# Kernel tuning notes

Hardware: AMD Instinct MI355X
Metric: run time of the kernel (lower is better)

Reference implementation:

```python
import jax, jax.numpy as jnp
import numpy as np

B, T, C = 2, 192, 512
H, D = 8, 64  # num_heads, head_dim; inner_dim = H*D = C


def setup_inputs() -> dict:
    key = jax.random.key(0)
    k1, k2, k3 = jax.random.split(key, 3)
    x = jax.random.normal(k1, (B, T, C), dtype=jnp.float32)
    W_in = jax.random.normal(k2, (C, 5 * H * D), dtype=jnp.float32) * 0.02
    b_in = jnp.zeros((5 * H * D,), dtype=jnp.float32)
    W_out = jax.random.normal(k3, (H * D, C), dtype=jnp.float32) * 0.02
    b_out = jnp.zeros((C,), dtype=jnp.float32)
    return {"x": x, "W_in": W_in, "b_in": b_in, "W_out": W_out, "b_out": b_out}


def _split_heads(t):
    # (B,T,H*D) -> (B,H,T,D)
    return t.reshape(B, T, H, D).transpose(0, 2, 1, 3)


def reference(x, W_in, b_in, W_out, b_out):
    scale = D ** -0.5
    proj = x @ W_in + b_in  # (B,T,5*H*D)
    q, k1, v1, k2, v2 = jnp.split(proj, 5, axis=-1)
    q = _split_heads(q) * scale
    k1 = _split_heads(k1)
    v1 = _split_heads(v1)
    k2 = _split_heads(k2)
    v2 = _split_heads(v2)
    # trilinear logits: <q_i, k1_j, k2_k> / sqrt(D), computed in fp32
    logits = jnp.einsum('bhid,bhjd,bhkd->bhijk', q, k1, k2,
                        preferred_element_type=jnp.float32)
    # softmax over the joint (j,k) axes
    attn = jax.nn.softmax(logits.reshape(B, H, T, T * T), axis=-1)
    attn = attn.reshape(B, H, T, T, T).astype(x.dtype)
    # out_i[d] = sum_{j,k} attn[i,j,k] * v1_j[d] * v2_k[d]
    out = jnp.einsum('bhijk,bhjd,bhkd->bhid', attn, v1, v2)
    y = out.transpose(0, 2, 1, 3).reshape(B, T, H * D)  # merge heads
    return y @ W_out + b_out
```

## Files before the change

kernel.cpp:

```cpp
#include <hip/hip_runtime.h>
#include <hip/hip_bf16.h>


typedef float  v4f __attribute__((ext_vector_type(4)));
typedef short  v8s __attribute__((ext_vector_type(8)));

__device__ __forceinline__ unsigned short f2bf(float f) {
  unsigned u = __float_as_uint(f);
  u += 0x7fffu + ((u >> 16) & 1u);
  return (unsigned short)(u >> 16);
}
__device__ __forceinline__ float bf2f(unsigned short b) {
  return __uint_as_float(((unsigned)b) << 16);
}
__device__ __forceinline__ unsigned pack_bf16(float lo, float hi) {
  __hip_bfloat162 t = __float22bfloat162_rn(float2{lo, hi});
  union { __hip_bfloat162 b; unsigned u; } cv;
  cv.b = t;
  return cv.u;
}

#if __has_builtin(__builtin_amdgcn_exp2f)
#define EXP2F(x) __builtin_amdgcn_exp2f(x)
#else
#define EXP2F(x) exp2f(x)
#endif

#define MFMA32(a, b, c) __builtin_amdgcn_mfma_f32_16x16x32_bf16((a), (b), (c), 0, 0, 0)

#define QSCALE 0.18033688011112042f


#define XH_OFF   589824
#define XL_OFF   786432
#define WTH_OFF  983040
#define WTL_OFF  2293760
#define WOTH_OFF 3604480
#define WOTL_OFF 3866624
#define OH_OFF   4128768
#define OL_OFF   4325376

__device__ __forceinline__ int v1perm(int t) {
  return (t & ~31) | (((t >> 2) & 3) << 3) | (((t >> 4) & 1) << 2) | (t & 3);
}

__global__ __launch_bounds__(256) void prep_kernel(
    const float* __restrict__ x, const float* __restrict__ Win,
    const float* __restrict__ Wout, unsigned short* __restrict__ wsh) {
  __shared__ float tile[32 * 65];
  const int bi = blockIdx.x, t = threadIdx.x;
  if (bi < 768) {
    const float* W; unsigned short *Th, *Tl; int R, n0, k0;
    if (bi < 640) {
      W = Win; Th = wsh + WTH_OFF; Tl = wsh + WTL_OFF; R = 2560;
      n0 = (bi % 40) << 6; k0 = (bi / 40) << 5;
    } else {
      const int idx = bi - 640;
      W = Wout; Th = wsh + WOTH_OFF; Tl = wsh + WOTL_OFF; R = 512;
      n0 = (idx & 7) << 6; k0 = (idx >> 3) << 5;
    }
    const int n = t & 63, kq = (t >> 6) * 8;
#pragma unroll
    for (int j = 0; j < 8; ++j)
      tile[(kq + j) * 65 + n] = W[(k0 + kq + j) * R + n0 + n];
    __syncthreads();
    const int n2 = t >> 2, ks = (t & 3) * 8;
    union { uint4 u; unsigned short us[8]; } ph, pl;
#pragma unroll
    for (int j = 0; j < 8; ++j) {
      const float v = tile[(ks + j) * 65 + n2];
      const unsigned short h = f2bf(v);
      ph.us[j] = h;
      pl.us[j] = f2bf(v - bf2f(h));
    }
    *(uint4*)(Th + (n0 + n2) * 512 + k0 + ks) = ph.u;
    *(uint4*)(Tl + (n0 + n2) * 512 + k0 + ks) = pl.u;
  } else {
    const int flat = ((bi - 768) * 256 + t) * 8;
    const v4f v0 = *(const v4f*)(x + flat);
    const v4f v1 = *(const v4f*)(x + flat + 4);
    union { uint4 u; unsigned short us[8]; } ph, pl;
#pragma unroll
    for (int j = 0; j < 4; ++j) {
      unsigned short h = f2bf(v0[j]);
      ph.us[j] = h; pl.us[j] = f2bf(v0[j] - bf2f(h));
      h = f2bf(v1[j]);
      ph.us[4 + j] = h; pl.us[4 + j] = f2bf(v1[j] - bf2f(h));
    }
    *(uint4*)(wsh + XH_OFF + flat) = ph.u;
    *(uint4*)(wsh + XL_OFF + flat) = pl.u;
  }
}

__global__ __launch_bounds__(64) void proj_kernel(
    const unsigned short* __restrict__ wsh, const float* __restrict__ bin,
    float* __restrict__ wsf, unsigned short* __restrict__ wshd) {
  const int lane = threadIdx.x;
  const int c = lane & 15, q = lane >> 4;
  const int bm = blockIdx.x % 12, bn = blockIdx.x / 12;

  const unsigned short* base[8];
  base[0] = wsh + XH_OFF + (bm * 32 + c) * 512 + (q << 3);
  base[1] = base[0] + 16 * 512;
  base[2] = wsh + XL_OFF + (bm * 32 + c) * 512 + (q << 3);
  base[3] = base[2] + 16 * 512;
  base[4] = wsh + WTH_OFF + (bn * 32 + c) * 512 + (q << 3);
  base[5] = base[4] + 16 * 512;
  base[6] = wsh + WTL_OFF + (bn * 32 + c) * 512 + (q << 3);
  base[7] = base[6] + 16 * 512;

  const v4f z = {0.f, 0.f, 0.f, 0.f};
  v4f a00 = z, a01 = z, a10 = z, a11 = z;

  v8s cur[8], nxt[8];
#pragma unroll
  for (int i = 0; i < 8; ++i) cur[i] = *(const v8s*)(base[i]);
#pragma unroll
  for (int i = 0; i < 8; ++i) nxt[i] = *(const v8s*)(base[i] + 32);

#pragma unroll 1
  for (int ks = 0; ks < 16; ++ks) {
    v8s nx2[8];
    if (ks < 14) {
      const int o = (ks + 2) * 32;
#pragma unroll
      for (int i = 0; i < 8; ++i) nx2[i] = *(const v8s*)(base[i] + o);
    }
    a00 = MFMA32(cur[2], cur[4], a00); a00 = MFMA32(cur[0], cur[6], a00); a00 = MFMA32(cur[0], cur[4], a00);
    a01 = MFMA32(cur[2], cur[5], a01); a01 = MFMA32(cur[0], cur[7], a01); a01 = MFMA32(cur[0], cur[5], a01);
    a10 = MFMA32(cur[3], cur[4], a10); a10 = MFMA32(cur[1], cur[6], a10); a10 = MFMA32(cur[1], cur[4], a10);
    a11 = MFMA32(cur[3], cur[5], a11); a11 = MFMA32(cur[1], cur[7], a11); a11 = MFMA32(cur[1], cur[5], a11);
#pragma unroll
    for (int i = 0; i < 8; ++i) { cur[i] = nxt[i]; nxt[i] = nx2[i]; }
  }

  v4f accs[2][2] = {{a00, a01}, {a10, a11}};
#pragma unroll
  for (int mt = 0; mt < 2; ++mt) {
#pragma unroll
    for (int nt = 0; nt < 2; ++nt) {
      const int n = bn * 32 + nt * 16 + c;
      const int which = n >> 9, cc = n & 511, h = cc >> 6, d = cc & 63;
      const float bv = bin[n];
#pragma unroll
      for (int r = 0; r < 4; ++r) {
        const int m = bm * 32 + mt * 16 + (q << 2) + r;
        const int b = (m >= 192) ? 1 : 0;
        const int tt = m - (b ? 192 : 0);
        const int bh = b * 8 + h;
        const float val = accs[mt][nt][r] + bv;
        const int rm = ((bh * 192 + tt) << 6) + d;
        if (which == 0)      wsf[rm] = val * QSCALE;
        else if (which == 1) wshd[rm] = f2bf(val);
        else if (which == 2) wshd[393216 + ((bh << 6) + d) * 192 + v1perm(tt)] = f2bf(val);
        else if (which == 3) wshd[196608 + rm] = f2bf(val);
        else wsf[196608 + ((bh * 192 + tt) << 6) + ((d >> 4) << 4) + (d & 15)] = val;
      }
    }
  }
}

__global__ __launch_bounds__(256, 2) void attn_kernel(
    const float* __restrict__ wsf, const unsigned short* __restrict__ wsh,
    float* __restrict__ accp, float* __restrict__ Sp) {
  __shared__ char smem[17408];
  unsigned short* K2s = (unsigned short*)smem;

  const int tid  = threadIdx.x;
  const int wv   = tid >> 6;
  const int lane = tid & 63;
  const int c    = lane & 15;
  const int quad = lane >> 4;
  const int jh   = wv & 1;
  const int kh   = wv >> 1;

  const int bb = blockIdx.x;
  const int kb = bb & 3;
  const int it = (bb >> 2) % 12;
  const int bh = bb / 48;

  const unsigned short* k1g = wsh + bh * 192 * 64;
  const unsigned short* v1g = wsh + 393216 + bh * 64 * 192;
  const unsigned short* k2g = wsh + 196608 + bh * 192 * 64;
  const float*          v2g = wsf + 196608 + bh * 12288;

  for (int idx = tid; idx < 384; idx += 256) {
    const int r = idx >> 3, c8 = (idx & 7) * 8;
    *(uint4*)(K2s + r * 64 + c8) = *(const uint4*)(k2g + (kb * 48 + r) * 64 + c8);
  }

  v8s k1f[6][2];
#pragma unroll
  for (int j = 0; j < 6; ++j) {
    const unsigned short* kp = k1g + (((jh * 6 + j) * 16 + c) << 6) + (quad << 3);
    k1f[j][0] = *(const v8s*)(kp);
    k1f[j][1] = *(const v8s*)(kp + 32);
  }

  v8s vf[3][4];
#pragma unroll
  for (int m = 0; m < 3; ++m)
#pragma unroll
    for (int dt = 0; dt < 4; ++dt)
      vf[m][dt] = *(const v8s*)(v1g + (dt * 16 + c) * 192 + ((jh * 3 + m) << 5) + (quad << 3));

  const float* qg = wsf + ((bh * 192 + it * 16 + c) << 6) + (quad << 3);
  float q0[8], q1[8];
  {
    v4f qa = *(const v4f*)(qg), qb = *(const v4f*)(qg + 4);
    v4f qc = *(const v4f*)(qg + 32), qd = *(const v4f*)(qg + 36);
#pragma unroll
    for (int e = 0; e < 4; ++e) {
      q0[e] = qa[e]; q0[4 + e] = qb[e];
      q1[e] = qc[e]; q1[4 + e] = qd[e];
    }
  }
  __syncthreads();

  const v4f z = {0.f, 0.f, 0.f, 0.f};
  v4f acc[4] = {z, z, z, z};
  float sS = 0.f;

  union U4 { uint4 u4; unsigned short us[8]; };
  union AF { v8s v; unsigned u[4]; };

#pragma unroll 1
  for (int ks = 0; ks < 24; ++ks) {
    const int rl = kh * 24 + ks;
    U4 kl, khh;
    kl.u4  = *(const uint4*)(K2s + (rl << 6) + (quad << 3));
    khh.u4 = *(const uint4*)(K2s + (rl << 6) + (quad << 3) + 32);
    const float* vb = v2g + ((kb * 48 + rl) << 6) + (quad << 2);
    const v4f vt0 = *(const v4f*)(vb);
    const v4f vt1 = *(const v4f*)(vb + 16);
    const v4f vt2 = *(const v4f*)(vb + 32);
    const v4f vt3 = *(const v4f*)(vb + 48);

    AF af0, af1;
#pragma unroll
    for (int e = 0; e < 4; ++e) {
      af0.u[e] = pack_bf16(q0[2*e] * bf2f(kl.us[2*e]),  q0[2*e+1] * bf2f(kl.us[2*e+1]));
      af1.u[e] = pack_bf16(q1[2*e] * bf2f(khh.us[2*e]), q1[2*e+1] * bf2f(khh.us[2*e+1]));
    }

    v4f o0 = z, o1 = z, o2 = z, o3 = z;
#pragma unroll
    for (int m = 0; m < 3; ++m) {
      v4f Ca = MFMA32(k1f[2*m][0],   af0.v, z);
      Ca = MFMA32(k1f[2*m][1],   af1.v, Ca);
      v4f Cb = MFMA32(k1f[2*m+1][0], af0.v, z);
      Cb = MFMA32(k1f[2*m+1][1], af1.v, Cb);
#pragma unroll
      for (int r = 0; r < 4; ++r) { Ca[r] = EXP2F(Ca[r]); Cb[r] = EXP2F(Cb[r]); }
      sS += Ca[0] + Ca[1] + Ca[2] + Ca[3] + Cb[0] + Cb[1] + Cb[2] + Cb[3];
      AF pp;
      pp.u[0] = pack_bf16(Ca[0], Ca[1]);
      pp.u[1] = pack_bf16(Ca[2], Ca[3]);
      pp.u[2] = pack_bf16(Cb[0], Cb[1]);
      pp.u[3] = pack_bf16(Cb[2], Cb[3]);
      o0 = MFMA32(vf[m][0], pp.v, o0);
      o1 = MFMA32(vf[m][1], pp.v, o1);
      o2 = MFMA32(vf[m][2], pp.v, o2);
      o3 = MFMA32(vf[m][3], pp.v, o3);
    }
    acc[0] += o0 * vt0;
    acc[1] += o1 * vt1;
    acc[2] += o2 * vt2;
    acc[3] += o3 * vt3;
  }

  __syncthreads();
  float* redA = (float*)smem;
  float* redS = (float*)smem + 4096;

#pragma unroll
  for (int dt = 0; dt < 4; ++dt)
    *(v4f*)(redA + wv * 1024 + (c << 6) + (dt << 4) + (quad << 2)) = acc[dt];
  redS[wv * 64 + (quad << 4) + c] = sS;
  __syncthreads();

  const int pbase = (bh * 12 + it) * 4 + kb;
  float* ap_out = accp + pbase * 1024;
  for (int idx = tid; idx < 1024; idx += 256)
    ap_out[idx] = redA[idx] + redA[1024 + idx] + redA[2048 + idx] + redA[3072 + idx];
  if (tid < 16) {
    float s = 0.f;
#pragma unroll
    for (int w = 0; w < 4; ++w)
#pragma unroll
      for (int qq = 0; qq < 4; ++qq)
        s += redS[w * 64 + qq * 16 + tid];
    Sp[pbase * 16 + tid] = s;
  }
}

__global__ __launch_bounds__(256) void norm_kernel(
    const float* __restrict__ accp, const float* __restrict__ Sp,
    unsigned short* __restrict__ wsh) {
  const int flat = blockIdx.x * 2048 + threadIdx.x * 8;
  const int m = flat >> 9, cc = flat & 511;
  const int b = (m >= 192) ? 1 : 0;
  const int tt = m - (b ? 192 : 0);
  const int h = cc >> 6, d0 = cc & 63;
  const int bh = b * 8 + h, it = tt >> 4, i = tt & 15;
  const int pb = (bh * 12 + it) * 4;
  const float* ap = accp + pb * 1024 + (i << 6) + d0;
  v4f a0 = *(const v4f*)(ap), a1 = *(const v4f*)(ap + 4);
  float Sv = Sp[pb * 16 + i];
#pragma unroll
  for (int kb = 1; kb < 4; ++kb) {
    a0 += *(const v4f*)(ap + kb * 1024);
    a1 += *(const v4f*)(ap + kb * 1024 + 4);
    Sv += Sp[(pb + kb) * 16 + i];
  }
  const float inv = 1.0f / Sv;
  union { uint4 u; unsigned short us[8]; } ph, pl;
#pragma unroll
  for (int j = 0; j < 4; ++j) {
    float v = a0[j] * inv;
    unsigned short hh = f2bf(v);
    ph.us[j] = hh; pl.us[j] = f2bf(v - bf2f(hh));
    v = a1[j] * inv;
    hh = f2bf(v);
    ph.us[4 + j] = hh; pl.us[4 + j] = f2bf(v - bf2f(hh));
  }
  *(uint4*)(wsh + OH_OFF + flat) = ph.u;
  *(uint4*)(wsh + OL_OFF + flat) = pl.u;
}

__global__ __launch_bounds__(64) void outp_kernel(
    const unsigned short* __restrict__ wsh, const float* __restrict__ bout,
    float* __restrict__ y) {
  const int lane = threadIdx.x;
  const int c = lane & 15, q = lane >> 4;
  const int bm = blockIdx.x % 12, bn = blockIdx.x / 12;

  const unsigned short* base[8];
  base[0] = wsh + OH_OFF + (bm * 32 + c) * 512 + (q << 3);
  base[1] = base[0] + 16 * 512;
  base[2] = wsh + OL_OFF + (bm * 32 + c) * 512 + (q << 3);
  base[3] = base[2] + 16 * 512;
  base[4] = wsh + WOTH_OFF + (bn * 32 + c) * 512 + (q << 3);
  base[5] = base[4] + 16 * 512;
  base[6] = wsh + WOTL_OFF + (bn * 32 + c) * 512 + (q << 3);
  base[7] = base[6] + 16 * 512;

  const v4f z = {0.f, 0.f, 0.f, 0.f};
  v4f a00 = z, a01 = z, a10 = z, a11 = z;

  v8s cur[8], nxt[8];
#pragma unroll
  for (int i = 0; i < 8; ++i) cur[i] = *(const v8s*)(base[i]);
#pragma unroll
  for (int i = 0; i < 8; ++i) nxt[i] = *(const v8s*)(base[i] + 32);

#pragma unroll 1
  for (int ks = 0; ks < 16; ++ks) {
    v8s nx2[8];
    if (ks < 14) {
      const int o = (ks + 2) * 32;
#pragma unroll
      for (int i = 0; i < 8; ++i) nx2[i] = *(const v8s*)(base[i] + o);
    }
    a00 = MFMA32(cur[2], cur[4], a00); a00 = MFMA32(cur[0], cur[6], a00); a00 = MFMA32(cur[0], cur[4], a00);
    a01 = MFMA32(cur[2], cur[5], a01); a01 = MFMA32(cur[0], cur[7], a01); a01 = MFMA32(cur[0], cur[5], a01);
    a10 = MFMA32(cur[3], cur[4], a10); a10 = MFMA32(cur[1], cur[6], a10); a10 = MFMA32(cur[1], cur[4], a10);
    a11 = MFMA32(cur[3], cur[5], a11); a11 = MFMA32(cur[1], cur[7], a11); a11 = MFMA32(cur[1], cur[5], a11);
#pragma unroll
    for (int i = 0; i < 8; ++i) { cur[i] = nxt[i]; nxt[i] = nx2[i]; }
  }

  v4f accs[2][2] = {{a00, a01}, {a10, a11}};
#pragma unroll
  for (int mt = 0; mt < 2; ++mt) {
#pragma unroll
    for (int nt = 0; nt < 2; ++nt) {
      const int n = bn * 32 + nt * 16 + c;
      const float bv = bout[n];
#pragma unroll
      for (int r = 0; r < 4; ++r) {
        const int m = bm * 32 + mt * 16 + (q << 2) + r;
        y[m * 512 + n] = accs[mt][nt][r] + bv;
      }
    }
  }
}

extern "C" void kernel_launch(void* const* d_in, const int* in_sizes, int n_in,
                              void* d_out, int out_size, void* d_ws, size_t ws_size,
                              hipStream_t stream) {
  const float* x    = (const float*)d_in[0];
  const float* Win  = (const float*)d_in[1];
  const float* bin  = (const float*)d_in[2];
  const float* Wout = (const float*)d_in[3];
  const float* bout = (const float*)d_in[4];

  float* wsf = (float*)d_ws;
  unsigned short* wsh = (unsigned short*)(wsf + 1191936);
  float* accp = wsf + 393216;
  float* Sp   = wsf + 1179648;

  prep_kernel<<<dim3(864), 256, 0, stream>>>(x, Win, Wout, wsh);
  proj_kernel<<<dim3(960), 64, 0, stream>>>(wsh, bin, wsf, wsh);
  attn_kernel<<<dim3(768), 256, 0, stream>>>(wsf, wsh, accp, Sp);
  norm_kernel<<<dim3(96), 256, 0, stream>>>(accp, Sp, wsh);
  outp_kernel<<<dim3(192), 64, 0, stream>>>(wsh, bout, (float*)d_out);
}
```

Measured before the change: 143.8 us.

## Stage projection epilogue through LDS, pre-convert K2 to fp32, sum softmax via MFMA

The projection epilogue now writes accumulators into a shared tile and stores coalesced vector rows, including a transposed and permuted V1 layout, instead of scattered scalar stores. The attention kernel converts K2 to fp32 once when staging it in shared memory, which removes the per-iteration bf16 unpack. It also computes the softmax denominator with an MFMA against a ones vector, replacing the VALU adds and the 4-way quad reduction. The trade-offs are twice the LDS traffic for K2, a softmax sum taken from bf16-rounded probabilities, and more live registers from restructuring all six logit tiles before the PV MFMAs.

```diff
diff --git a/kernel.cpp b/kernel.cpp
--- a/kernel.cpp
+++ b/kernel.cpp
@@ -40,8 +40,8 @@
 #define OH_OFF   4128768
 #define OL_OFF   4325376
 
-__device__ __forceinline__ int v1perm(int t) {
-  return (t & ~31) | (((t >> 2) & 3) << 3) | (((t >> 4) & 1) << 2) | (t & 3);
+__device__ __forceinline__ int v1perm_inv(int p) {
+  return (((p >> 3) & 3) << 2) | (((p >> 2) & 1) << 4) | (p & 3);
 }
 
 __global__ __launch_bounds__(256) void prep_kernel(
@@ -95,6 +95,7 @@
 __global__ __launch_bounds__(64) void proj_kernel(
     const unsigned short* __restrict__ wsh, const float* __restrict__ bin,
     float* __restrict__ wsf, unsigned short* __restrict__ wshd) {
+  __shared__ float tile[32 * 33];
   const int lane = threadIdx.x;
   const int c = lane & 15, q = lane >> 4;
   const int bm = blockIdx.x % 12, bn = blockIdx.x / 12;
@@ -134,28 +135,58 @@
     for (int i = 0; i < 8; ++i) { cur[i] = nxt[i]; nxt[i] = nx2[i]; }
   }
 
+  const int n0 = bn * 32;
+  const int which = n0 >> 9;
+  const int h  = (n0 & 511) >> 6;
+  const int d0 = n0 & 63;
+  const int b  = (bm >= 6) ? 1 : 0;
+  const int bh = b * 8 + h;
+  const int tt0 = (bm - b * 6) * 32;
+
   v4f accs[2][2] = {{a00, a01}, {a10, a11}};
 #pragma unroll
-  for (int mt = 0; mt < 2; ++mt) {
+  for (int mt = 0; mt < 2; ++mt)
 #pragma unroll
     for (int nt = 0; nt < 2; ++nt) {
-      const int n = bn * 32 + nt * 16 + c;
-      const int which = n >> 9, cc = n & 511, h = cc >> 6, d = cc & 63;
-      const float bv = bin[n];
-#pragma unroll
-      for (int r = 0; r < 4; ++r) {
-        const int m = bm * 32 + mt * 16 + (q << 2) + r;
-        const int b = (m >= 192) ? 1 : 0;
-        const int tt = m - (b ? 192 : 0);
-        const int bh = b * 8 + h;
-        const float val = accs[mt][nt][r] + bv;
-        const int rm = ((bh * 192 + tt) << 6) + d;
-        if (which == 0)      wsf[rm] = val * QSCALE;
-        else if (which == 1) wshd[rm] = f2bf(val);
-        else if (which == 2) wshd[393216 + ((bh << 6) + d) * 192 + v1perm(tt)] = f2bf(val);
-        else if (which == 3) wshd[196608 + rm] = f2bf(val);
-        else wsf[196608 + ((bh * 192 + tt) << 6) + ((d >> 4) << 4) + (d & 15)] = val;
+      const float bv = bin[n0 + nt * 16 + c];
+#pragma unroll
+      for (int r = 0; r < 4; ++r)
+        tile[(mt * 16 + (q << 2) + r) * 33 + nt * 16 + c] = accs[mt][nt][r] + bv;
+    }
+  __syncthreads();
+
+  const int rr = lane >> 1, cc0 = (lane & 1) * 16;
+  if (which == 0 || which == 4) {
+    float* out = wsf + (which == 4 ? 196608 : 0) + ((bh * 192 + tt0 + rr) << 6) + d0 + cc0;
+    const float s = (which == 0) ? QSCALE : 1.0f;
+#pragma unroll
+    for (int i = 0; i < 16; i += 4) {
+      v4f v;
+#pragma unroll
+      for (int j = 0; j < 4; ++j) v[j] = tile[rr * 33 + cc0 + i + j] * s;
+      *(v4f*)(out + i) = v;
+    }
+  } else if (which == 1 || which == 3) {
+    unsigned short* out = wshd + (which == 3 ? 196608 : 0) + ((bh * 192 + tt0 + rr) << 6) + d0 + cc0;
+#pragma unroll
+    for (int hf = 0; hf < 2; ++hf) {
+      union { uint4 u; unsigned short us[8]; } pk;
+#pragma unroll
+      for (int j = 0; j < 8; ++j) pk.us[j] = f2bf(tile[rr * 33 + cc0 + hf * 8 + j]);
+      *(uint4*)(out + hf * 8) = pk.u;
+    }
+  } else {
+    const int dd = rr, p0 = cc0;
+    unsigned short* out = wshd + 393216 + ((bh << 6) + d0 + dd) * 192 + tt0 + p0;
+#pragma unroll
+    for (int hf = 0; hf < 2; ++hf) {
+      union { uint4 u; unsigned short us[8]; } pk;
+#pragma unroll
+      for (int j = 0; j < 8; ++j) {
+        const int p = p0 + hf * 8 + j;
+        pk.us[j] = f2bf(tile[v1perm_inv(p) * 33 + dd]);
       }
+      *(uint4*)(out + hf * 8) = pk.u;
     }
   }
 }
@@ -164,7 +195,7 @@
     const float* __restrict__ wsf, const unsigned short* __restrict__ wsh,
     float* __restrict__ accp, float* __restrict__ Sp) {
   __shared__ char smem[17408];
-  unsigned short* K2s = (unsigned short*)smem;
+  float* K2f = (float*)smem;
 
   const int tid  = threadIdx.x;
   const int wv   = tid >> 6;
@@ -186,7 +217,13 @@
 
   for (int idx = tid; idx < 384; idx += 256) {
     const int r = idx >> 3, c8 = (idx & 7) * 8;
-    *(uint4*)(K2s + r * 64 + c8) = *(const uint4*)(k2g + (kb * 48 + r) * 64 + c8);
+    union { uint4 u4; unsigned short us[8]; } t;
+    t.u4 = *(const uint4*)(k2g + (kb * 48 + r) * 64 + c8);
+    v4f lo, hi;
+#pragma unroll
+    for (int e = 0; e < 4; ++e) { lo[e] = bf2f(t.us[e]); hi[e] = bf2f(t.us[4 + e]); }
+    *(v4f*)(K2f + r * 64 + c8)     = lo;
+    *(v4f*)(K2f + r * 64 + c8 + 4) = hi;
   }
 
   v8s k1f[6][2];
@@ -219,17 +256,20 @@
 
   const v4f z = {0.f, 0.f, 0.f, 0.f};
   v4f acc[4] = {z, z, z, z};
-  float sS = 0.f;
-
-  union U4 { uint4 u4; unsigned short us[8]; };
+  v4f oS = z;
+  const short one = (short)0x3F80;
+  const v8s ones = {one, one, one, one, one, one, one, one};
+
   union AF { v8s v; unsigned u[4]; };
 
 #pragma unroll 1
   for (int ks = 0; ks < 24; ++ks) {
     const int rl = kh * 24 + ks;
-    U4 kl, khh;
-    kl.u4  = *(const uint4*)(K2s + (rl << 6) + (quad << 3));
-    khh.u4 = *(const uint4*)(K2s + (rl << 6) + (quad << 3) + 32);
+    const float* kp = K2f + (rl << 6) + (quad << 3);
+    const v4f k2a = *(const v4f*)(kp);
+    const v4f k2b = *(const v4f*)(kp + 4);
+    const v4f k2c = *(const v4f*)(kp + 32);
+    const v4f k2d = *(const v4f*)(kp + 36);
     const float* vb = v2g + ((kb * 48 + rl) << 6) + (quad << 2);
     const v4f vt0 = *(const v4f*)(vb);
     const v4f vt1 = *(const v4f*)(vb + 16);
@@ -237,31 +277,42 @@
     const v4f vt3 = *(const v4f*)(vb + 48);
 
     AF af0, af1;
-#pragma unroll
-    for (int e = 0; e < 4; ++e) {
-      af0.u[e] = pack_bf16(q0[2*e] * bf2f(kl.us[2*e]),  q0[2*e+1] * bf2f(kl.us[2*e+1]));
-      af1.u[e] = pack_bf16(q1[2*e] * bf2f(khh.us[2*e]), q1[2*e+1] * bf2f(khh.us[2*e+1]));
-    }
-
+    af0.u[0] = pack_bf16(q0[0] * k2a[0], q0[1] * k2a[1]);
+    af0.u[1] = pack_bf16(q0[2] * k2a[2], q0[3] * k2a[3]);
+    af0.u[2] = pack_bf16(q0[4] * k2b[0], q0[5] * k2b[1]);
+    af0.u[3] = pack_bf16(q0[6] * k2b[2], q0[7] * k2b[3]);
+    af1.u[0] = pack_bf16(q1[0] * k2c[0], q1[1] * k2c[1]);
+    af1.u[1] = pack_bf16(q1[2] * k2c[2], q1[3] * k2c[3]);
+    af1.u[2] = pack_bf16(q1[4] * k2d[0], q1[5] * k2d[1]);
+    af1.u[3] = pack_bf16(q1[6] * k2d[2], q1[7] * k2d[3]);
+
+    v4f C[6];
+#pragma unroll
+    for (int jj = 0; jj < 6; ++jj) {
+      v4f t0 = MFMA32(k1f[jj][0], af0.v, z);
+      C[jj] = MFMA32(k1f[jj][1], af1.v, t0);
+    }
+#pragma unroll
+    for (int jj = 0; jj < 6; ++jj)
+#pragma unroll
+      for (int r = 0; r < 4; ++r) C[jj][r] = EXP2F(C[jj][r]);
+    AF pp[3];
+#pragma unroll
+    for (int m = 0; m < 3; ++m) {
+      pp[m].u[0] = pack_bf16(C[2*m][0],   C[2*m][1]);
+      pp[m].u[1] = pack_bf16(C[2*m][2],   C[2*m][3]);
+      pp[m].u[2] = pack_bf16(C[2*m+1][0], C[2*m+1][1]);
+      pp[m].u[3] = pack_bf16(C[2*m+1][2], C[2*m+1][3]);
+    }
+#pragma unroll
+    for (int m = 0; m < 3; ++m) oS = MFMA32(ones, pp[m].v, oS);
     v4f o0 = z, o1 = z, o2 = z, o3 = z;
 #pragma unroll
     for (int m = 0; m < 3; ++m) {
-      v4f Ca = MFMA32(k1f[2*m][0],   af0.v, z);
-      Ca = MFMA32(k1f[2*m][1],   af1.v, Ca);
-      v4f Cb = MFMA32(k1f[2*m+1][0], af0.v, z);
-      Cb = MFMA32(k1f[2*m+1][1], af1.v, Cb);
-#pragma unroll
-      for (int r = 0; r < 4; ++r) { Ca[r] = EXP2F(Ca[r]); Cb[r] = EXP2F(Cb[r]); }
-      sS += Ca[0] + Ca[1] + Ca[2] + Ca[3] + Cb[0] + Cb[1] + Cb[2] + Cb[3];
-      AF pp;
-      pp.u[0] = pack_bf16(Ca[0], Ca[1]);
-      pp.u[1] = pack_bf16(Ca[2], Ca[3]);
-      pp.u[2] = pack_bf16(Cb[0], Cb[1]);
-      pp.u[3] = pack_bf16(Cb[2], Cb[3]);
-      o0 = MFMA32(vf[m][0], pp.v, o0);
-      o1 = MFMA32(vf[m][1], pp.v, o1);
-      o2 = MFMA32(vf[m][2], pp.v, o2);
-      o3 = MFMA32(vf[m][3], pp.v, o3);
+      o0 = MFMA32(vf[m][0], pp[m].v, o0);
+      o1 = MFMA32(vf[m][1], pp[m].v, o1);
+      o2 = MFMA32(vf[m][2], pp[m].v, o2);
+      o3 = MFMA32(vf[m][3], pp[m].v, o3);
     }
     acc[0] += o0 * vt0;
     acc[1] += o1 * vt1;
@@ -276,22 +327,15 @@
 #pragma unroll
   for (int dt = 0; dt < 4; ++dt)
     *(v4f*)(redA + wv * 1024 + (c << 6) + (dt << 4) + (quad << 2)) = acc[dt];
-  redS[wv * 64 + (quad << 4) + c] = sS;
+  if (quad == 0) redS[wv * 16 + c] = oS[0];
   __syncthreads();
 
   const int pbase = (bh * 12 + it) * 4 + kb;
   float* ap_out = accp + pbase * 1024;
   for (int idx = tid; idx < 1024; idx += 256)
     ap_out[idx] = redA[idx] + redA[1024 + idx] + redA[2048 + idx] + redA[3072 + idx];
-  if (tid < 16) {
-    float s = 0.f;
-#pragma unroll
-    for (int w = 0; w < 4; ++w)
-#pragma unroll
-      for (int qq = 0; qq < 4; ++qq)
-        s += redS[w * 64 + qq * 16 + tid];
-    Sp[pbase * 16 + tid] = s;
-  }
+  if (tid < 16)
+    Sp[pbase * 16 + tid] = redS[tid] + redS[16 + tid] + redS[32 + tid] + redS[48 + tid];
 }
 
 __global__ __launch_bounds__(256) void norm_kernel(
```

Result: no change. 146.5 us (+1.9%).

## Fuse softmax normalization into output projection and coalesce projection epilogue stores

Applied to the files above, without the earlier changes.

Merges the separate normalization kernel into the output-projection GEMM: each block reduces the partial accumulators, divides by the softmax denominator, splits into bf16 hi/lo in shared memory, then runs MFMAs against Wout. This removes one launch and the global round trip for the normalized activations, at the cost of fewer, larger blocks (48). The projection epilogue now stages its tile in shared memory so Q/K/V writes (including the permuted V1 transpose) become vectorized, coalesced stores instead of scattered scalar ones. The attention inner loop unroll is raised to 2.

```diff
diff --git a/kernel.cpp b/kernel.cpp
--- a/kernel.cpp
+++ b/kernel.cpp
@@ -37,11 +37,9 @@
 #define WTL_OFF  2293760
 #define WOTH_OFF 3604480
 #define WOTL_OFF 3866624
-#define OH_OFF   4128768
-#define OL_OFF   4325376
-
-__device__ __forceinline__ int v1perm(int t) {
-  return (t & ~31) | (((t >> 2) & 3) << 3) | (((t >> 4) & 1) << 2) | (t & 3);
+
+__device__ __forceinline__ int v1perm_inv(int p) {
+  return (((p >> 3) & 3) << 2) | (((p >> 2) & 1) << 4) | (p & 3);
 }
 
 __global__ __launch_bounds__(256) void prep_kernel(
@@ -95,6 +93,7 @@
 __global__ __launch_bounds__(64) void proj_kernel(
     const unsigned short* __restrict__ wsh, const float* __restrict__ bin,
     float* __restrict__ wsf, unsigned short* __restrict__ wshd) {
+  __shared__ float tile[32 * 33];
   const int lane = threadIdx.x;
   const int c = lane & 15, q = lane >> 4;
   const int bm = blockIdx.x % 12, bn = blockIdx.x / 12;
@@ -134,28 +133,58 @@
     for (int i = 0; i < 8; ++i) { cur[i] = nxt[i]; nxt[i] = nx2[i]; }
   }
 
+  const int n0 = bn * 32;
+  const int which = n0 >> 9;
+  const int h  = (n0 & 511) >> 6;
+  const int d0 = n0 & 63;
+  const int b  = (bm >= 6) ? 1 : 0;
+  const int bh = b * 8 + h;
+  const int tt0 = (bm - b * 6) * 32;
+
   v4f accs[2][2] = {{a00, a01}, {a10, a11}};
 #pragma unroll
-  for (int mt = 0; mt < 2; ++mt) {
+  for (int mt = 0; mt < 2; ++mt)
 #pragma unroll
     for (int nt = 0; nt < 2; ++nt) {
-      const int n = bn * 32 + nt * 16 + c;
-      const int which = n >> 9, cc = n & 511, h = cc >> 6, d = cc & 63;
-      const float bv = bin[n];
-#pragma unroll
-      for (int r = 0; r < 4; ++r) {
-        const int m = bm * 32 + mt * 16 + (q << 2) + r;
-        const int b = (m >= 192) ? 1 : 0;
-        const int tt = m - (b ? 192 : 0);
-        const int bh = b * 8 + h;
-        const float val = accs[mt][nt][r] + bv;
-        const int rm = ((bh * 192 + tt) << 6) + d;
-        if (which == 0)      wsf[rm] = val * QSCALE;
-        else if (which == 1) wshd[rm] = f2bf(val);
-        else if (which == 2) wshd[393216 + ((bh << 6) + d) * 192 + v1perm(tt)] = f2bf(val);
-        else if (which == 3) wshd[196608 + rm] = f2bf(val);
-        else wsf[196608 + ((bh * 192 + tt) << 6) + ((d >> 4) << 4) + (d & 15)] = val;
+      const float bv = bin[n0 + nt * 16 + c];
+#pragma unroll
+      for (int r = 0; r < 4; ++r)
+        tile[(mt * 16 + (q << 2) + r) * 33 + nt * 16 + c] = accs[mt][nt][r] + bv;
+    }
+  __syncthreads();
+
+  const int rr = lane >> 1, cc0 = (lane & 1) * 16;
+  if (which == 0 || which == 4) {
+    float* out = wsf + (which == 4 ? 196608 : 0) + ((bh * 192 + tt0 + rr) << 6) + d0 + cc0;
+    const float s = (which == 0) ? QSCALE : 1.0f;
+#pragma unroll
+    for (int i = 0; i < 16; i += 4) {
+      v4f v;
+#pragma unroll
+      for (int j = 0; j < 4; ++j) v[j] = tile[rr * 33 + cc0 + i + j] * s;
+      *(v4f*)(out + i) = v;
+    }
+  } else if (which == 1 || which == 3) {
+    unsigned short* out = wshd + (which == 3 ? 196608 : 0) + ((bh * 192 + tt0 + rr) << 6) + d0 + cc0;
+#pragma unroll
+    for (int hf = 0; hf < 2; ++hf) {
+      union { uint4 u; unsigned short us[8]; } pk;
+#pragma unroll
+      for (int j = 0; j < 8; ++j) pk.us[j] = f2bf(tile[rr * 33 + cc0 + hf * 8 + j]);
+      *(uint4*)(out + hf * 8) = pk.u;
+    }
+  } else {
+    const int dd = rr, p0 = cc0;
+    unsigned short* out = wshd + 393216 + ((bh << 6) + d0 + dd) * 192 + tt0 + p0;
+#pragma unroll
+    for (int hf = 0; hf < 2; ++hf) {
+      union { uint4 u; unsigned short us[8]; } pk;
+#pragma unroll
+      for (int j = 0; j < 8; ++j) {
+        const int p = p0 + hf * 8 + j;
+        pk.us[j] = f2bf(tile[v1perm_inv(p) * 33 + dd]);
       }
+      *(uint4*)(out + hf * 8) = pk.u;
     }
   }
 }
@@ -224,7 +253,7 @@
   union U4 { uint4 u4; unsigned short us[8]; };
   union AF { v8s v; unsigned u[4]; };
 
-#pragma unroll 1
+#pragma unroll 2
   for (int ks = 0; ks < 24; ++ks) {
     const int rl = kh * 24 + ks;
     U4 kl, khh;
@@ -294,95 +323,91 @@
   }
 }
 
-__global__ __launch_bounds__(256) void norm_kernel(
-    const float* __restrict__ accp, const float* __restrict__ Sp,
-    unsigned short* __restrict__ wsh) {
-  const int flat = blockIdx.x * 2048 + threadIdx.x * 8;
-  const int m = flat >> 9, cc = flat & 511;
-  const int b = (m >= 192) ? 1 : 0;
-  const int tt = m - (b ? 192 : 0);
-  const int h = cc >> 6, d0 = cc & 63;
-  const int bh = b * 8 + h, it = tt >> 4, i = tt & 15;
-  const int pb = (bh * 12 + it) * 4;
-  const float* ap = accp + pb * 1024 + (i << 6) + d0;
-  v4f a0 = *(const v4f*)(ap), a1 = *(const v4f*)(ap + 4);
-  float Sv = Sp[pb * 16 + i];
-#pragma unroll
-  for (int kb = 1; kb < 4; ++kb) {
-    a0 += *(const v4f*)(ap + kb * 1024);
-    a1 += *(const v4f*)(ap + kb * 1024 + 4);
-    Sv += Sp[(pb + kb) * 16 + i];
-  }
-  const float inv = 1.0f / Sv;
-  union { uint4 u; unsigned short us[8]; } ph, pl;
-#pragma unroll
-  for (int j = 0; j < 4; ++j) {
-    float v = a0[j] * inv;
-    unsigned short hh = f2bf(v);
-    ph.us[j] = hh; pl.us[j] = f2bf(v - bf2f(hh));
-    v = a1[j] * inv;
-    hh = f2bf(v);
-    ph.us[4 + j] = hh; pl.us[4 + j] = f2bf(v - bf2f(hh));
-  }
-  *(uint4*)(wsh + OH_OFF + flat) = ph.u;
-  *(uint4*)(wsh + OL_OFF + flat) = pl.u;
-}
-
-__global__ __launch_bounds__(64) void outp_kernel(
-    const unsigned short* __restrict__ wsh, const float* __restrict__ bout,
-    float* __restrict__ y) {
-  const int lane = threadIdx.x;
+__global__ __launch_bounds__(256) void outp2_kernel(
+    const float* __restrict__ wsf, const unsigned short* __restrict__ wsh,
+    const float* __restrict__ bout, float* __restrict__ y) {
+  __shared__ unsigned short OHs[16 * 520];
+  __shared__ unsigned short OLs[16 * 520];
+  const float* accp = wsf + 393216;
+  const float* Sp   = wsf + 1179648;
+
+  const int tid = threadIdx.x;
+  const int nh  = blockIdx.x & 1;
+  const int bit = blockIdx.x >> 1;
+  const int b = bit / 12, it = bit % 12;
+  const int m0 = b * 192 + it * 16;
+
+  {
+    const int i = tid >> 4, cc0 = (tid & 15) * 32;
+    const int h = cc0 >> 6;
+    const int pb = ((b * 8 + h) * 12 + it) * 4;
+    const float inv = 1.0f / (Sp[pb * 16 + i] + Sp[(pb + 1) * 16 + i] +
+                              Sp[(pb + 2) * 16 + i] + Sp[(pb + 3) * 16 + i]);
+    const float* ap = accp + pb * 1024 + (i << 6) + (cc0 & 63);
+#pragma unroll
+    for (int g = 0; g < 8; ++g) {
+      v4f a = *(const v4f*)(ap + g * 4);
+      a += *(const v4f*)(ap + 1024 + g * 4);
+      a += *(const v4f*)(ap + 2048 + g * 4);
+      a += *(const v4f*)(ap + 3072 + g * 4);
+#pragma unroll
+      for (int j = 0; j < 4; ++j) {
+        const float v = a[j] * inv;
+        const unsigned short hh = f2bf(v);
+        OHs[i * 520 + cc0 + g * 4 + j] = hh;
+        OLs[i * 520 + cc0 + g * 4 + j] = f2bf(v - bf2f(hh));
+      }
+    }
+  }
+  __syncthreads();
+
+  const int lane = tid & 63, wv = tid >> 6;
   const int c = lane & 15, q = lane >> 4;
-  const int bm = blockIdx.x % 12, bn = blockIdx.x / 12;
-
-  const unsigned short* base[8];
-  base[0] = wsh + OH_OFF + (bm * 32 + c) * 512 + (q << 3);
-  base[1] = base[0] + 16 * 512;
-  base[2] = wsh + OL_OFF + (bm * 32 + c) * 512 + (q << 3);
-  base[3] = base[2] + 16 * 512;
-  base[4] = wsh + WOTH_OFF + (bn * 32 + c) * 512 + (q << 3);
-  base[5] = base[4] + 16 * 512;
-  base[6] = wsh + WOTL_OFF + (bn * 32 + c) * 512 + (q << 3);
-  base[7] = base[6] + 16 * 512;
-
+  const int n0w = nh * 256 + wv * 64;
   const v4f z = {0.f, 0.f, 0.f, 0.f};
-  v4f a00 = z, a01 = z, a10 = z, a11 = z;
-
-  v8s cur[8], nxt[8];
-#pragma unroll
-  for (int i = 0; i < 8; ++i) cur[i] = *(const v8s*)(base[i]);
-#pragma unroll
-  for (int i = 0; i < 8; ++i) nxt[i] = *(const v8s*)(base[i] + 32);
+  v4f acc[4] = {z, z, z, z};
+
+  const unsigned short* Bhb = wsh + WOTH_OFF;
+  const unsigned short* Blb = wsh + WOTL_OFF;
+
+  v8s cBh[4], cBl[4], nBh[4], nBl[4];
+#pragma unroll
+  for (int nt = 0; nt < 4; ++nt) {
+    const int n = n0w + nt * 16 + c;
+    cBh[nt] = *(const v8s*)(Bhb + n * 512 + (q << 3));
+    cBl[nt] = *(const v8s*)(Blb + n * 512 + (q << 3));
+  }
 
 #pragma unroll 1
   for (int ks = 0; ks < 16; ++ks) {
-    v8s nx2[8];
-    if (ks < 14) {
-      const int o = (ks + 2) * 32;
-#pragma unroll
-      for (int i = 0; i < 8; ++i) nx2[i] = *(const v8s*)(base[i] + o);
-    }
-    a00 = MFMA32(cur[2], cur[4], a00); a00 = MFMA32(cur[0], cur[6], a00); a00 = MFMA32(cur[0], cur[4], a00);
-    a01 = MFMA32(cur[2], cur[5], a01); a01 = MFMA32(cur[0], cur[7], a01); a01 = MFMA32(cur[0], cur[5], a01);
-    a10 = MFMA32(cur[3], cur[4], a10); a10 = MFMA32(cur[1], cur[6], a10); a10 = MFMA32(cur[1], cur[4], a10);
-    a11 = MFMA32(cur[3], cur[5], a11); a11 = MFMA32(cur[1], cur[7], a11); a11 = MFMA32(cur[1], cur[5], a11);
-#pragma unroll
-    for (int i = 0; i < 8; ++i) { cur[i] = nxt[i]; nxt[i] = nx2[i]; }
-  }
-
-  v4f accs[2][2] = {{a00, a01}, {a10, a11}};
-#pragma unroll
-  for (int mt = 0; mt < 2; ++mt) {
-#pragma unroll
-    for (int nt = 0; nt < 2; ++nt) {
-      const int n = bn * 32 + nt * 16 + c;
-      const float bv = bout[n];
-#pragma unroll
-      for (int r = 0; r < 4; ++r) {
-        const int m = bm * 32 + mt * 16 + (q << 2) + r;
-        y[m * 512 + n] = accs[mt][nt][r] + bv;
+    if (ks < 15) {
+      const int o = (ks + 1) * 32 + (q << 3);
+#pragma unroll
+      for (int nt = 0; nt < 4; ++nt) {
+        const int n = n0w + nt * 16 + c;
+        nBh[nt] = *(const v8s*)(Bhb + n * 512 + o);
+        nBl[nt] = *(const v8s*)(Blb + n * 512 + o);
       }
     }
+    const v8s Ah = *(const v8s*)(OHs + c * 520 + ks * 32 + (q << 3));
+    const v8s Al = *(const v8s*)(OLs + c * 520 + ks * 32 + (q << 3));
+#pragma unroll
+    for (int nt = 0; nt < 4; ++nt) {
+      acc[nt] = MFMA32(Al, cBh[nt], acc[nt]);
+      acc[nt] = MFMA32(Ah, cBl[nt], acc[nt]);
+      acc[nt] = MFMA32(Ah, cBh[nt], acc[nt]);
+    }
+#pragma unroll
+    for (int nt = 0; nt < 4; ++nt) { cBh[nt] = nBh[nt]; cBl[nt] = nBl[nt]; }
+  }
+
+#pragma unroll
+  for (int nt = 0; nt < 4; ++nt) {
+    const int n = n0w + nt * 16 + c;
+    const float bv = bout[n];
+#pragma unroll
+    for (int r = 0; r < 4; ++r)
+      y[(m0 + (q << 2) + r) * 512 + n] = acc[nt][r] + bv;
   }
 }
 
@@ -403,6 +428,5 @@
   prep_kernel<<<dim3(864), 256, 0, stream>>>(x, Win, Wout, wsh);
   proj_kernel<<<dim3(960), 64, 0, stream>>>(wsh, bin, wsf, wsh);
   attn_kernel<<<dim3(768), 256, 0, stream>>>(wsf, wsh, accp, Sp);
-  norm_kernel<<<dim3(96), 256, 0, stream>>>(accp, Sp, wsh);
-  outp_kernel<<<dim3(192), 64, 0, stream>>>(wsh, bout, (float*)d_out);
-}
+  outp2_kernel<<<dim3(48), 256, 0, stream>>>(wsf, wsh, bout, (float*)d_out);
+}
```

Result: slower. 151.7 us (+5.5%).
